# Optimization experiments

Hardware: AMD Instinct MI355X
Metric: run time of the kernel (lower is better)

## Reference

```python
import jax, jax.numpy as jnp
import numpy as np

EMB = 768
HEADS = 12
B, N = 8, 1024


def setup_inputs() -> dict:
    key = jax.random.key(0)
    ks = jax.random.split(key, 5)
    x = jax.random.normal(ks[0], (B, N, EMB), dtype=jnp.float32)
    # torch Linear params expressed as (in, out) matrices: y = x @ W + b
    W_qkv = jax.random.normal(ks[1], (EMB, 3 * EMB), dtype=jnp.float32) * (EMB ** -0.5)
    b_qkv = jax.random.normal(ks[2], (3 * EMB,), dtype=jnp.float32) * 0.02
    W_proj = jax.random.normal(ks[3], (EMB, EMB), dtype=jnp.float32) * (EMB ** -0.5)
    b_proj = jax.random.normal(ks[4], (EMB,), dtype=jnp.float32) * 0.02
    return {"x": x, "W_qkv": W_qkv, "b_qkv": b_qkv, "W_proj": W_proj, "b_proj": b_proj}


def reference(x, W_qkv, b_qkv, W_proj, b_proj):
    b, n, e = x.shape
    h = HEADS
    d = e // h
    qkv = x @ W_qkv + b_qkv                      # (b, n, 3e)
    # rearrange 'b n (h d qkv) -> qkv b h n d': qkv is the INNERMOST factor
    qkv = qkv.reshape(b, n, h, d, 3)
    q = jnp.transpose(qkv[..., 0], (0, 2, 1, 3))  # (b, h, n, d)
    k = jnp.transpose(qkv[..., 1], (0, 2, 1, 3))
    v = jnp.transpose(qkv[..., 2], (0, 2, 1, 3))
    energy = jnp.einsum('bhqd,bhkd->bhqk', q, k)  # UNscaled scores
    # faithful to source: softmax first, THEN divide by sqrt(emb_size)
    att = jax.nn.softmax(energy, axis=-1) / jnp.sqrt(jnp.float32(e))
    out = jnp.einsum('bhql,bhld->bhqd', att, v)   # (b, h, n, d)
    out = jnp.transpose(out, (0, 2, 1, 3)).reshape(b, n, e)
    return out @ W_proj + b_proj
```

## Files before the change

kernel.cpp:

```cpp
#include <hip/hip_runtime.h>
#include <hip/hip_bf16.h>
#include <stdint.h>

#define EMB 768
#define HEADS 12
#define BATCH 8
#define SEQ 1024
#define HD 64
#define M_ROWS (BATCH * SEQ)
#define QKV_COLS (3 * EMB)

typedef __attribute__((ext_vector_type(8))) short short8;
typedef __attribute__((ext_vector_type(4))) float f32x4;

__device__ __forceinline__ unsigned short f2bf(float x) {
    union { float f; unsigned u; } v; v.f = x;
    unsigned r = v.u + 0x7FFFu + ((v.u >> 16) & 1u);
    return (unsigned short)(r >> 16);
}
__device__ __forceinline__ float bf2f(unsigned short h) {
    union { unsigned u; float f; } v; v.u = ((unsigned)h) << 16;
    return v.f;
}
__device__ __forceinline__ float truncbf(float x) {
    return __uint_as_float(__float_as_uint(x) & 0xFFFF0000u);
}
__device__ __forceinline__ uint32_t packtr(float a, float b) {
    return (__float_as_uint(a) >> 16) | (__float_as_uint(b) & 0xFFFF0000u);
}
__device__ __forceinline__ uint32_t cvtpk(float a, float b) {
    uint32_t r;
    asm("v_cvt_pk_bf16_f32 %0, %1, %2" : "=v"(r) : "v"(a), "v"(b));
    return r;
}

#define MFMA16(a, b, c) __builtin_amdgcn_mfma_f32_16x16x32_bf16((a), (b), (c), 0, 0, 0)

__global__ __launch_bounds__(256)
void split_tw(const float* __restrict__ W,
              unsigned short* __restrict__ Wht, unsigned short* __restrict__ Wlt)
{
    __shared__ unsigned short Th[64][72], Tl[64][72];
    const int tid = threadIdx.x;
    const int ct = blockIdx.x * 64;
    const int kt = blockIdx.y * 64;

    #pragma unroll
    for (int p = 0; p < 4; ++p) {
        int idx = (p << 8) + tid;
        int k = idx >> 4, c4 = (idx & 15) << 2;
        f32x4 v = *reinterpret_cast<const f32x4*>(W + (size_t)(kt + k) * QKV_COLS + ct + c4);
        #pragma unroll
        for (int j = 0; j < 4; ++j) {
            const int whichj = (ct + c4 + j) % 3;
            if (whichj == 2) {
                Th[c4 + j][k] = f2bf(v[j]);
                Tl[c4 + j][k] = 0;
            } else {
                Th[c4 + j][k] = (unsigned short)(__float_as_uint(v[j]) >> 16);
                Tl[c4 + j][k] = (unsigned short)(__float_as_uint(v[j] - truncbf(v[j])) >> 16);
            }
        }
    }
    __syncthreads();
    #pragma unroll
    for (int p = 0; p < 2; ++p) {
        int idx = (p << 8) + tid;
        int c = idx >> 3, k8 = (idx & 7) << 3;
        const int s = ct + c;
        const int dst = (s % 3) * 768 + (s / 192) * 64 + (s % 192) / 3;
        *reinterpret_cast<uint4*>(Wht + (size_t)dst * EMB + kt + k8) =
            *reinterpret_cast<const uint4*>(&Th[c][k8]);
        *reinterpret_cast<uint4*>(Wlt + (size_t)dst * EMB + kt + k8) =
            *reinterpret_cast<const uint4*>(&Tl[c][k8]);
    }
}

__global__ __launch_bounds__(256, 2)
void gemm_qk(const float* __restrict__ X,
             const unsigned short* __restrict__ Wht, const unsigned short* __restrict__ Wlt,
             const float* __restrict__ bias,
             unsigned short* __restrict__ Qh, unsigned short* __restrict__ Ql,
             unsigned short* __restrict__ Kh, unsigned short* __restrict__ Kl)
{
    __shared__ unsigned short Ash[128][40], Asl[128][40];
    __shared__ unsigned short Bsh[128][40], Bsl[128][40];

    const int tid  = threadIdx.x;
    const int wave = tid >> 6, lane = tid & 63;
    const int lr = lane & 15, lg = lane >> 4;
    const int wr = (wave >> 1) * 64, wc = (wave & 1) * 64;
    const int m0 = blockIdx.y * 128;
    const int c0 = blockIdx.x * 128;

    const f32x4 fzero = {0.f, 0.f, 0.f, 0.f};
    f32x4 acc[4][4];
    #pragma unroll
    for (int m = 0; m < 4; ++m)
        #pragma unroll
        for (int n = 0; n < 4; ++n) acc[m][n] = fzero;

    for (int k0 = 0; k0 < EMB; k0 += 32) {
        #pragma unroll
        for (int p = 0; p < 4; ++p) {
            int idx = (p << 8) + tid;
            int row = idx >> 3, kc = (idx & 7) << 2;
            f32x4 v = *reinterpret_cast<const f32x4*>(X + (size_t)(m0 + row) * EMB + k0 + kc);
            float l0 = v[0] - truncbf(v[0]), l1 = v[1] - truncbf(v[1]);
            float l2 = v[2] - truncbf(v[2]), l3 = v[3] - truncbf(v[3]);
            uint2 hw = { packtr(v[0], v[1]), packtr(v[2], v[3]) };
            uint2 lw = { packtr(l0, l1), packtr(l2, l3) };
            *reinterpret_cast<uint2*>(&Ash[row][kc]) = hw;
            *reinterpret_cast<uint2*>(&Asl[row][kc]) = lw;
        }
        #pragma unroll
        for (int p = 0; p < 2; ++p) {
            int idx = (p << 8) + tid;
            int row = idx >> 2, kc = (idx & 3) << 3;
            const size_t boff = (size_t)(c0 + row) * EMB + k0 + kc;
            *reinterpret_cast<uint4*>(&Bsh[row][kc]) = *reinterpret_cast<const uint4*>(Wht + boff);
            *reinterpret_cast<uint4*>(&Bsl[row][kc]) = *reinterpret_cast<const uint4*>(Wlt + boff);
        }
        __syncthreads();

        short8 ah[4], al[4], bh[4], bl[4];
        #pragma unroll
        for (int m = 0; m < 4; ++m) {
            ah[m] = *reinterpret_cast<const short8*>(&Ash[wr + m * 16 + lr][lg << 3]);
            al[m] = *reinterpret_cast<const short8*>(&Asl[wr + m * 16 + lr][lg << 3]);
        }
        #pragma unroll
        for (int n = 0; n < 4; ++n) {
            bh[n] = *reinterpret_cast<const short8*>(&Bsh[wc + n * 16 + lr][lg << 3]);
            bl[n] = *reinterpret_cast<const short8*>(&Bsl[wc + n * 16 + lr][lg << 3]);
        }
        #pragma unroll
        for (int m = 0; m < 4; ++m)
            #pragma unroll
            for (int n = 0; n < 4; ++n) {
                acc[m][n] = MFMA16(ah[m], bh[n], acc[m][n]);
                acc[m][n] = MFMA16(ah[m], bl[n], acc[m][n]);
                acc[m][n] = MFMA16(al[m], bh[n], acc[m][n]);
            }
        __syncthreads();
    }

    const int which = c0 / 768;
    unsigned short* __restrict__ Ph = (which == 0) ? Qh : Kh;
    unsigned short* __restrict__ Pl = (which == 0) ? Ql : Kl;
    #pragma unroll
    for (int m = 0; m < 4; ++m) {
        #pragma unroll
        for (int n = 0; n < 4; ++n) {
            const int colg = c0 + wc + n * 16 + lr;
            const int hd = colg - which * 768;
            const int h  = hd >> 6;
            const int dd = hd & 63;
            const float bv = bias[192 * h + 3 * dd + which];
            const int rowg0 = m0 + wr + m * 16 + (lg << 2);
            const int bi = rowg0 >> 10, ni0 = rowg0 & (SEQ - 1);
            const int bhid = bi * HEADS + h;
            #pragma unroll
            for (int j = 0; j < 4; ++j) {
                const float val = acc[m][n][j] + bv;
                const size_t oidx = ((size_t)bhid * SEQ + ni0 + j) * HD + dd;
                const uint32_t uv = __float_as_uint(val);
                Ph[oidx] = (unsigned short)(uv >> 16);
                Pl[oidx] = (unsigned short)(__float_as_uint(
                    val - __uint_as_float(uv & 0xFFFF0000u)) >> 16);
            }
        }
    }
}

__global__ __launch_bounds__(256, 2)
void gemm_v(const float* __restrict__ X,
            const unsigned short* __restrict__ Wht,
            const float* __restrict__ bias,
            unsigned short* __restrict__ Vt)
{
    __shared__ unsigned short Ash[128][40];
    __shared__ unsigned short Bsh[128][40];

    const int tid  = threadIdx.x;
    const int wave = tid >> 6, lane = tid & 63;
    const int lr = lane & 15, lg = lane >> 4;
    const int wr = (wave >> 1) * 64, wc = (wave & 1) * 64;
    const int m0 = blockIdx.y * 128;
    const int c0 = blockIdx.x * 128;

    const f32x4 fzero = {0.f, 0.f, 0.f, 0.f};
    f32x4 acc[4][4];
    #pragma unroll
    for (int m = 0; m < 4; ++m)
        #pragma unroll
        for (int n = 0; n < 4; ++n) acc[m][n] = fzero;

    for (int k0 = 0; k0 < EMB; k0 += 32) {
        #pragma unroll
        for (int p = 0; p < 4; ++p) {
            int idx = (p << 8) + tid;
            int row = idx >> 3, kc = (idx & 7) << 2;
            f32x4 v = *reinterpret_cast<const f32x4*>(X + (size_t)(m0 + row) * EMB + k0 + kc);
            uint2 hw = { packtr(v[0], v[1]), packtr(v[2], v[3]) };
            *reinterpret_cast<uint2*>(&Ash[row][kc]) = hw;
        }
        #pragma unroll
        for (int p = 0; p < 2; ++p) {
            int idx = (p << 8) + tid;
            int row = idx >> 2, kc = (idx & 3) << 3;
            const size_t boff = (size_t)(1536 + c0 + row) * EMB + k0 + kc;
            *reinterpret_cast<uint4*>(&Bsh[row][kc]) = *reinterpret_cast<const uint4*>(Wht + boff);
        }
        __syncthreads();

        short8 a[4], b[4];
        #pragma unroll
        for (int m = 0; m < 4; ++m)
            a[m] = *reinterpret_cast<const short8*>(&Ash[wr + m * 16 + lr][lg << 3]);
        #pragma unroll
        for (int n = 0; n < 4; ++n)
            b[n] = *reinterpret_cast<const short8*>(&Bsh[wc + n * 16 + lr][lg << 3]);
        #pragma unroll
        for (int m = 0; m < 4; ++m)
            #pragma unroll
            for (int n = 0; n < 4; ++n)
                acc[m][n] = MFMA16(a[m], b[n], acc[m][n]);
        __syncthreads();
    }

    #pragma unroll
    for (int m = 0; m < 4; ++m) {
        #pragma unroll
        for (int n = 0; n < 4; ++n) {
            const int hd = c0 + wc + n * 16 + lr;
            const int h  = hd >> 6;
            const int dd = hd & 63;
            const float bv = bias[192 * h + 3 * dd + 2];
            const int rowg0 = m0 + wr + m * 16 + (lg << 2);
            const int bi = rowg0 >> 10, ni0 = rowg0 & (SEQ - 1);
            const int bhid = bi * HEADS + h;
            const float v0 = acc[m][n][0] + bv, v1 = acc[m][n][1] + bv;
            const float v2 = acc[m][n][2] + bv, v3 = acc[m][n][3] + bv;
            uint2 w = { (uint32_t)f2bf(v0) | ((uint32_t)f2bf(v1) << 16),
                        (uint32_t)f2bf(v2) | ((uint32_t)f2bf(v3) << 16) };
            *reinterpret_cast<uint2*>(Vt + ((size_t)bhid * HD + dd) * SEQ + ni0) = w;
        }
    }
}

__global__ __launch_bounds__(256, 4)
void attn_fused(const unsigned short* __restrict__ Qh, const unsigned short* __restrict__ Ql,
                const unsigned short* __restrict__ Kh, const unsigned short* __restrict__ Kl,
                const unsigned short* __restrict__ Vt,
                unsigned short* __restrict__ Ob)
{
    __shared__ unsigned short Vs[64][72];
    __shared__ unsigned short Ksh[64][72];
    __shared__ unsigned short Ksl[64][72];
    __shared__ unsigned short Plds[4][16][72];

    const int tid  = threadIdx.x;
    const int wave = tid >> 6, lane = tid & 63;
    const int lr = lane & 15, lg = lane >> 4;

    const int bid = blockIdx.x;
    const int lid = (bid & 7) * 192 + (bid >> 3);
    const int qt = lid & 15;
    const int bh = lid >> 4;
    const int b = bh / HEADS, h = bh % HEADS;

    const size_t base = (size_t)bh * SEQ * HD;
    const unsigned short* Qhb = Qh + base;
    const unsigned short* Qlb = Ql + base;
    const unsigned short* Khb = Kh + base;
    const unsigned short* Klb = Kl + base;
    const unsigned short* Vtb = Vt + base;

    const int q0 = qt * 64 + wave * 16;

    short8 qh[2], ql[2];
    #pragma unroll
    for (int kk = 0; kk < 2; ++kk) {
        const size_t off = (size_t)(q0 + lr) * HD + kk * 32 + (lg << 3);
        qh[kk] = *reinterpret_cast<const short8*>(Qhb + off);
        ql[kk] = *reinterpret_cast<const short8*>(Qlb + off);
    }

    const int r0 = tid >> 3, cs = (tid & 7) << 3;
    const int r1 = r0 + 32;

    uint4 vr0 = *reinterpret_cast<const uint4*>(Vtb + (size_t)r0 * SEQ + cs);
    uint4 vr1 = *reinterpret_cast<const uint4*>(Vtb + (size_t)r1 * SEQ + cs);
    uint4 kh0 = *reinterpret_cast<const uint4*>(Khb + (size_t)r0 * HD + cs);
    uint4 kh1 = *reinterpret_cast<const uint4*>(Khb + (size_t)r1 * HD + cs);
    uint4 kl0 = *reinterpret_cast<const uint4*>(Klb + (size_t)r0 * HD + cs);
    uint4 kl1 = *reinterpret_cast<const uint4*>(Klb + (size_t)r1 * HD + cs);

    float m = -1.0e30f, l = 0.f;
    f32x4 oacc[4];
    const f32x4 fzero = {0.f, 0.f, 0.f, 0.f};
    #pragma unroll
    for (int d = 0; d < 4; ++d) oacc[d] = fzero;

    for (int t = 0; t < SEQ / 64; ++t) {
        __syncthreads();
        *reinterpret_cast<uint4*>(&Vs[r0][cs])  = vr0;
        *reinterpret_cast<uint4*>(&Vs[r1][cs])  = vr1;
        *reinterpret_cast<uint4*>(&Ksh[r0][cs]) = kh0;
        *reinterpret_cast<uint4*>(&Ksh[r1][cs]) = kh1;
        *reinterpret_cast<uint4*>(&Ksl[r0][cs]) = kl0;
        *reinterpret_cast<uint4*>(&Ksl[r1][cs]) = kl1;
        __syncthreads();

        if (t < SEQ / 64 - 1) {
            const int kb = (t + 1) * 64;
            vr0 = *reinterpret_cast<const uint4*>(Vtb + (size_t)r0 * SEQ + kb + cs);
            vr1 = *reinterpret_cast<const uint4*>(Vtb + (size_t)r1 * SEQ + kb + cs);
            kh0 = *reinterpret_cast<const uint4*>(Khb + (size_t)(kb + r0) * HD + cs);
            kh1 = *reinterpret_cast<const uint4*>(Khb + (size_t)(kb + r1) * HD + cs);
            kl0 = *reinterpret_cast<const uint4*>(Klb + (size_t)(kb + r0) * HD + cs);
            kl1 = *reinterpret_cast<const uint4*>(Klb + (size_t)(kb + r1) * HD + cs);
        }

        f32x4 s[4];
        #pragma unroll
        for (int n = 0; n < 4; ++n) s[n] = fzero;
        #pragma unroll
        for (int n = 0; n < 4; ++n) {
            #pragma unroll
            for (int kk = 0; kk < 2; ++kk) {
                const short8 kh = *reinterpret_cast<const short8*>(&Ksh[n * 16 + lr][kk * 32 + (lg << 3)]);
                const short8 kl = *reinterpret_cast<const short8*>(&Ksl[n * 16 + lr][kk * 32 + (lg << 3)]);
                s[n] = MFMA16(kh, qh[kk], s[n]);
                s[n] = MFMA16(kh, ql[kk], s[n]);
                s[n] = MFMA16(kl, qh[kk], s[n]);
            }
        }

        float a0 = fmaxf(fmaxf(s[0][0], s[0][1]), s[0][2]);
        float a1 = fmaxf(fmaxf(s[0][3], s[1][0]), s[1][1]);
        float a2 = fmaxf(fmaxf(s[1][2], s[1][3]), s[2][0]);
        float a3 = fmaxf(fmaxf(s[2][1], s[2][2]), s[2][3]);
        float a4 = fmaxf(fmaxf(s[3][0], s[3][1]), s[3][2]);
        float tmax = fmaxf(fmaxf(fmaxf(a0, a1), a2), fmaxf(fmaxf(a3, a4), s[3][3]));
        tmax = fmaxf(tmax, __shfl_xor(tmax, 16));
        tmax = fmaxf(tmax, __shfl_xor(tmax, 32));

        if (!__all(tmax <= m + 8.0f)) {
            const float mnew = fmaxf(m, tmax);
            const float corr = __expf(m - mnew);
            m = mnew;
            l *= corr;
            #pragma unroll
            for (int j = 0; j < 4; ++j) {
                const float cj = __shfl(corr, (lg << 2) + j);
                oacc[0][j] *= cj; oacc[1][j] *= cj;
                oacc[2][j] *= cj; oacc[3][j] *= cj;
            }
        }

        float psum = 0.f;
        #pragma unroll
        for (int n = 0; n < 4; ++n) {
            const float p0 = __expf(s[n][0] - m), p1 = __expf(s[n][1] - m);
            const float p2 = __expf(s[n][2] - m), p3 = __expf(s[n][3] - m);
            psum += (p0 + p1) + (p2 + p3);
            uint2 w = { cvtpk(p0, p1), cvtpk(p2, p3) };
            *reinterpret_cast<uint2*>(&Plds[wave][lr][n * 16 + (lg << 2)]) = w;
        }
        psum += __shfl_xor(psum, 16);
        psum += __shfl_xor(psum, 32);
        l += psum;

        #pragma unroll
        for (int kk = 0; kk < 2; ++kk) {
            const short8 ap = *reinterpret_cast<const short8*>(&Plds[wave][lr][kk * 32 + (lg << 3)]);
            #pragma unroll
            for (int d = 0; d < 4; ++d) {
                const short8 bv = *reinterpret_cast<const short8*>(&Vs[d * 16 + lr][kk * 32 + (lg << 3)]);
                oacc[d] = MFMA16(ap, bv, oacc[d]);
            }
        }
    }

    const float rs = 0.036084391824351615f;
    #pragma unroll
    for (int j = 0; j < 4; ++j) {
        const float lj = __shfl(l, (lg << 2) + j);
        const float sc = rs / lj;
        const int q = q0 + (lg << 2) + j;
        #pragma unroll
        for (int d = 0; d < 4; ++d) {
            const float val = oacc[d][j] * sc;
            Ob[((size_t)b * SEQ + q) * EMB + h * HD + d * 16 + lr] = f2bf(val);
        }
    }
}

__global__ __launch_bounds__(256, 4)
void gemm_proj(const unsigned short* __restrict__ A, const float* __restrict__ W,
               const float* __restrict__ bias, float* __restrict__ Out)
{
    __shared__ unsigned short As[128][40];
    __shared__ unsigned short Bs[128][40];

    const int tid  = threadIdx.x;
    const int wave = tid >> 6, lane = tid & 63;
    const int lr = lane & 15, lg = lane >> 4;
    const int wr = (wave >> 1) * 64, wc = (wave & 1) * 64;
    const int m0 = blockIdx.y * 128;
    const int c0 = blockIdx.x * 128;

    const f32x4 fzero = {0.f, 0.f, 0.f, 0.f};
    f32x4 acc[4][4];
    #pragma unroll
    for (int m = 0; m < 4; ++m)
        #pragma unroll
        for (int n = 0; n < 4; ++n) acc[m][n] = fzero;

    const int kgB = tid & 7, cgB = tid >> 3;

    for (int k0 = 0; k0 < EMB; k0 += 32) {
        #pragma unroll
        for (int p = 0; p < 2; ++p) {
            int idx = (p << 8) + tid;
            int row = idx >> 2, kc = (idx & 3) << 3;
            uint4 v = *reinterpret_cast<const uint4*>(A + (size_t)(m0 + row) * EMB + k0 + kc);
            *reinterpret_cast<uint4*>(&As[row][kc]) = v;
        }
        {
            f32x4 v[4];
            #pragma unroll
            for (int i = 0; i < 4; ++i)
                v[i] = *reinterpret_cast<const f32x4*>(
                    W + (size_t)(k0 + kgB * 4 + i) * EMB + c0 + cgB * 4);
            #pragma unroll
            for (int j = 0; j < 4; ++j) {
                uint2 w = { (uint32_t)f2bf(v[0][j]) | ((uint32_t)f2bf(v[1][j]) << 16),
                            (uint32_t)f2bf(v[2][j]) | ((uint32_t)f2bf(v[3][j]) << 16) };
                *reinterpret_cast<uint2*>(&Bs[cgB * 4 + j][kgB * 4]) = w;
            }
        }
        __syncthreads();

        short8 a[4], b[4];
        #pragma unroll
        for (int m = 0; m < 4; ++m)
            a[m] = *reinterpret_cast<const short8*>(&As[wr + m * 16 + lr][lg << 3]);
        #pragma unroll
        for (int n = 0; n < 4; ++n)
            b[n] = *reinterpret_cast<const short8*>(&Bs[wc + n * 16 + lr][lg << 3]);
        #pragma unroll
        for (int m = 0; m < 4; ++m)
            #pragma unroll
            for (int n = 0; n < 4; ++n)
                acc[m][n] = MFMA16(a[m], b[n], acc[m][n]);
        __syncthreads();
    }

    #pragma unroll
    for (int m = 0; m < 4; ++m) {
        #pragma unroll
        for (int n = 0; n < 4; ++n) {
            const int colg = c0 + wc + n * 16 + lr;
            const float bv = bias[colg];
            #pragma unroll
            for (int j = 0; j < 4; ++j) {
                const int rowg = m0 + wr + m * 16 + (lg << 2) + j;
                Out[(size_t)rowg * EMB + colg] = acc[m][n][j] + bv;
            }
        }
    }
}

extern "C" void kernel_launch(void* const* d_in, const int* in_sizes, int n_in,
                              void* d_out, int out_size, void* d_ws, size_t ws_size,
                              hipStream_t stream)
{
    const float* x     = (const float*)d_in[0];
    const float* Wqkv  = (const float*)d_in[1];
    const float* bqkv  = (const float*)d_in[2];
    const float* Wproj = (const float*)d_in[3];
    const float* bproj = (const float*)d_in[4];
    float* out = (float*)d_out;

    const size_t NQ = (size_t)BATCH * HEADS * SEQ * HD;
    const size_t NW = (size_t)EMB * QKV_COLS;

    unsigned short* Qh = (unsigned short*)d_ws;
    unsigned short* Ql = Qh + NQ;
    unsigned short* Kh = Ql + NQ;
    unsigned short* Kl = Kh + NQ;
    unsigned short* Vt = Kl + NQ;
    unsigned short* Ob = Vt + NQ;

    unsigned short* Wht = Ob;
    unsigned short* Wlt = Wht + NW;

    split_tw<<<dim3(QKV_COLS / 64, EMB / 64), 256, 0, stream>>>(Wqkv, Wht, Wlt);
    gemm_qk<<<dim3(1536 / 128, M_ROWS / 128), 256, 0, stream>>>(
        x, Wht, Wlt, bqkv, Qh, Ql, Kh, Kl);
    gemm_v<<<dim3(768 / 128, M_ROWS / 128), 256, 0, stream>>>(
        x, Wht, bqkv, Vt);
    attn_fused<<<dim3(16 * BATCH * HEADS), 256, 0, stream>>>(Qh, Ql, Kh, Kl, Vt, Ob);
    gemm_proj<<<dim3(EMB / 128, M_ROWS / 128), 256, 0, stream>>>(
        Ob, Wproj, bproj, out);
}
```

Baseline: 207.0 us.

## Process two query tiles per attention block and double QK GEMM K-step

The attention kernel now handles 128 queries per block as two 64-query sub-tiles, so each K/V tile staged in shared memory is reused by twice as many queries and the grid is halved. Each sub-tile keeps its own online-softmax state and P buffer. The QK projection GEMM moves from 32 to 64 k-elements per iteration with larger LDS tiles, which halves the number of barrier pairs. In exchange both kernels use more registers and LDS, occupancy drops (attention launch bounds go from 4 to 3), and the attention grid has fewer blocks to spread across the CUs.

Result: no change. 210.9 us (+1.9%).

```diff
diff --git a/kernel.cpp b/kernel.cpp
--- a/kernel.cpp
+++ b/kernel.cpp
@@ -83,8 +83,8 @@
              unsigned short* __restrict__ Qh, unsigned short* __restrict__ Ql,
              unsigned short* __restrict__ Kh, unsigned short* __restrict__ Kl)
 {
-    __shared__ unsigned short Ash[128][40], Asl[128][40];
-    __shared__ unsigned short Bsh[128][40], Bsl[128][40];
+    __shared__ unsigned short Ash[128][72], Asl[128][72];
+    __shared__ unsigned short Bsh[128][72], Bsl[128][72];
 
     const int tid  = threadIdx.x;
     const int wave = tid >> 6, lane = tid & 63;
@@ -100,11 +100,11 @@
         #pragma unroll
         for (int n = 0; n < 4; ++n) acc[m][n] = fzero;
 
-    for (int k0 = 0; k0 < EMB; k0 += 32) {
-        #pragma unroll
-        for (int p = 0; p < 4; ++p) {
+    for (int k0 = 0; k0 < EMB; k0 += 64) {
+        #pragma unroll
+        for (int p = 0; p < 8; ++p) {
             int idx = (p << 8) + tid;
-            int row = idx >> 3, kc = (idx & 7) << 2;
+            int row = idx >> 4, kc = (idx & 15) << 2;
             f32x4 v = *reinterpret_cast<const f32x4*>(X + (size_t)(m0 + row) * EMB + k0 + kc);
             float l0 = v[0] - truncbf(v[0]), l1 = v[1] - truncbf(v[1]);
             float l2 = v[2] - truncbf(v[2]), l3 = v[3] - truncbf(v[3]);
@@ -114,34 +114,37 @@
             *reinterpret_cast<uint2*>(&Asl[row][kc]) = lw;
         }
         #pragma unroll
-        for (int p = 0; p < 2; ++p) {
+        for (int p = 0; p < 4; ++p) {
             int idx = (p << 8) + tid;
-            int row = idx >> 2, kc = (idx & 3) << 3;
+            int row = idx >> 3, kc = (idx & 7) << 3;
             const size_t boff = (size_t)(c0 + row) * EMB + k0 + kc;
             *reinterpret_cast<uint4*>(&Bsh[row][kc]) = *reinterpret_cast<const uint4*>(Wht + boff);
             *reinterpret_cast<uint4*>(&Bsl[row][kc]) = *reinterpret_cast<const uint4*>(Wlt + boff);
         }
         __syncthreads();
 
-        short8 ah[4], al[4], bh[4], bl[4];
-        #pragma unroll
-        for (int m = 0; m < 4; ++m) {
-            ah[m] = *reinterpret_cast<const short8*>(&Ash[wr + m * 16 + lr][lg << 3]);
-            al[m] = *reinterpret_cast<const short8*>(&Asl[wr + m * 16 + lr][lg << 3]);
-        }
-        #pragma unroll
-        for (int n = 0; n < 4; ++n) {
-            bh[n] = *reinterpret_cast<const short8*>(&Bsh[wc + n * 16 + lr][lg << 3]);
-            bl[n] = *reinterpret_cast<const short8*>(&Bsl[wc + n * 16 + lr][lg << 3]);
-        }
-        #pragma unroll
-        for (int m = 0; m < 4; ++m)
+        #pragma unroll
+        for (int kk = 0; kk < 2; ++kk) {
+            short8 ah[4], al[4], bh[4], bl[4];
+            #pragma unroll
+            for (int m = 0; m < 4; ++m) {
+                ah[m] = *reinterpret_cast<const short8*>(&Ash[wr + m * 16 + lr][kk * 32 + (lg << 3)]);
+                al[m] = *reinterpret_cast<const short8*>(&Asl[wr + m * 16 + lr][kk * 32 + (lg << 3)]);
+            }
             #pragma unroll
             for (int n = 0; n < 4; ++n) {
-                acc[m][n] = MFMA16(ah[m], bh[n], acc[m][n]);
-                acc[m][n] = MFMA16(ah[m], bl[n], acc[m][n]);
-                acc[m][n] = MFMA16(al[m], bh[n], acc[m][n]);
-            }
+                bh[n] = *reinterpret_cast<const short8*>(&Bsh[wc + n * 16 + lr][kk * 32 + (lg << 3)]);
+                bl[n] = *reinterpret_cast<const short8*>(&Bsl[wc + n * 16 + lr][kk * 32 + (lg << 3)]);
+            }
+            #pragma unroll
+            for (int m = 0; m < 4; ++m)
+                #pragma unroll
+                for (int n = 0; n < 4; ++n) {
+                    acc[m][n] = MFMA16(ah[m], bh[n], acc[m][n]);
+                    acc[m][n] = MFMA16(ah[m], bl[n], acc[m][n]);
+                    acc[m][n] = MFMA16(al[m], bh[n], acc[m][n]);
+                }
+        }
         __syncthreads();
     }
 
@@ -249,7 +252,7 @@
     }
 }
 
-__global__ __launch_bounds__(256, 4)
+__global__ __launch_bounds__(256, 3)
 void attn_fused(const unsigned short* __restrict__ Qh, const unsigned short* __restrict__ Ql,
                 const unsigned short* __restrict__ Kh, const unsigned short* __restrict__ Kl,
                 const unsigned short* __restrict__ Vt,
@@ -258,16 +261,16 @@
     __shared__ unsigned short Vs[64][72];
     __shared__ unsigned short Ksh[64][72];
     __shared__ unsigned short Ksl[64][72];
-    __shared__ unsigned short Plds[4][16][72];
+    __shared__ unsigned short Plds[2][4][16][72];
 
     const int tid  = threadIdx.x;
     const int wave = tid >> 6, lane = tid & 63;
     const int lr = lane & 15, lg = lane >> 4;
 
     const int bid = blockIdx.x;
-    const int lid = (bid & 7) * 192 + (bid >> 3);
-    const int qt = lid & 15;
-    const int bh = lid >> 4;
+    const int lid = (bid & 7) * 96 + (bid >> 3);
+    const int qt = lid & 7;
+    const int bh = lid >> 3;
     const int b = bh / HEADS, h = bh % HEADS;
 
     const size_t base = (size_t)bh * SEQ * HD;
@@ -277,14 +280,18 @@
     const unsigned short* Klb = Kl + base;
     const unsigned short* Vtb = Vt + base;
 
-    const int q0 = qt * 64 + wave * 16;
-
-    short8 qh[2], ql[2];
+    const int qA = qt * 128 + wave * 16;
+    const int qB = qA + 64;
+
+    short8 qhA[2], qlA[2], qhB[2], qlB[2];
     #pragma unroll
     for (int kk = 0; kk < 2; ++kk) {
-        const size_t off = (size_t)(q0 + lr) * HD + kk * 32 + (lg << 3);
-        qh[kk] = *reinterpret_cast<const short8*>(Qhb + off);
-        ql[kk] = *reinterpret_cast<const short8*>(Qlb + off);
+        const size_t offA = (size_t)(qA + lr) * HD + kk * 32 + (lg << 3);
+        const size_t offB = (size_t)(qB + lr) * HD + kk * 32 + (lg << 3);
+        qhA[kk] = *reinterpret_cast<const short8*>(Qhb + offA);
+        qlA[kk] = *reinterpret_cast<const short8*>(Qlb + offA);
+        qhB[kk] = *reinterpret_cast<const short8*>(Qhb + offB);
+        qlB[kk] = *reinterpret_cast<const short8*>(Qlb + offB);
     }
 
     const int r0 = tid >> 3, cs = (tid & 7) << 3;
@@ -297,11 +304,11 @@
     uint4 kl0 = *reinterpret_cast<const uint4*>(Klb + (size_t)r0 * HD + cs);
     uint4 kl1 = *reinterpret_cast<const uint4*>(Klb + (size_t)r1 * HD + cs);
 
-    float m = -1.0e30f, l = 0.f;
-    f32x4 oacc[4];
+    float mA = -1.0e30f, lA = 0.f, mB = -1.0e30f, lB = 0.f;
+    f32x4 oaccA[4], oaccB[4];
     const f32x4 fzero = {0.f, 0.f, 0.f, 0.f};
     #pragma unroll
-    for (int d = 0; d < 4; ++d) oacc[d] = fzero;
+    for (int d = 0; d < 4; ++d) { oaccA[d] = fzero; oaccB[d] = fzero; }
 
     for (int t = 0; t < SEQ / 64; ++t) {
         __syncthreads();
@@ -323,63 +330,109 @@
             kl1 = *reinterpret_cast<const uint4*>(Klb + (size_t)(kb + r1) * HD + cs);
         }
 
-        f32x4 s[4];
-        #pragma unroll
-        for (int n = 0; n < 4; ++n) s[n] = fzero;
+        f32x4 sA[4], sB[4];
+        #pragma unroll
+        for (int n = 0; n < 4; ++n) { sA[n] = fzero; sB[n] = fzero; }
         #pragma unroll
         for (int n = 0; n < 4; ++n) {
             #pragma unroll
             for (int kk = 0; kk < 2; ++kk) {
                 const short8 kh = *reinterpret_cast<const short8*>(&Ksh[n * 16 + lr][kk * 32 + (lg << 3)]);
                 const short8 kl = *reinterpret_cast<const short8*>(&Ksl[n * 16 + lr][kk * 32 + (lg << 3)]);
-                s[n] = MFMA16(kh, qh[kk], s[n]);
-                s[n] = MFMA16(kh, ql[kk], s[n]);
-                s[n] = MFMA16(kl, qh[kk], s[n]);
-            }
-        }
-
-        float a0 = fmaxf(fmaxf(s[0][0], s[0][1]), s[0][2]);
-        float a1 = fmaxf(fmaxf(s[0][3], s[1][0]), s[1][1]);
-        float a2 = fmaxf(fmaxf(s[1][2], s[1][3]), s[2][0]);
-        float a3 = fmaxf(fmaxf(s[2][1], s[2][2]), s[2][3]);
-        float a4 = fmaxf(fmaxf(s[3][0], s[3][1]), s[3][2]);
-        float tmax = fmaxf(fmaxf(fmaxf(a0, a1), a2), fmaxf(fmaxf(a3, a4), s[3][3]));
-        tmax = fmaxf(tmax, __shfl_xor(tmax, 16));
-        tmax = fmaxf(tmax, __shfl_xor(tmax, 32));
-
-        if (!__all(tmax <= m + 8.0f)) {
-            const float mnew = fmaxf(m, tmax);
-            const float corr = __expf(m - mnew);
-            m = mnew;
-            l *= corr;
-            #pragma unroll
-            for (int j = 0; j < 4; ++j) {
-                const float cj = __shfl(corr, (lg << 2) + j);
-                oacc[0][j] *= cj; oacc[1][j] *= cj;
-                oacc[2][j] *= cj; oacc[3][j] *= cj;
-            }
-        }
-
-        float psum = 0.f;
-        #pragma unroll
-        for (int n = 0; n < 4; ++n) {
-            const float p0 = __expf(s[n][0] - m), p1 = __expf(s[n][1] - m);
-            const float p2 = __expf(s[n][2] - m), p3 = __expf(s[n][3] - m);
-            psum += (p0 + p1) + (p2 + p3);
-            uint2 w = { cvtpk(p0, p1), cvtpk(p2, p3) };
-            *reinterpret_cast<uint2*>(&Plds[wave][lr][n * 16 + (lg << 2)]) = w;
-        }
-        psum += __shfl_xor(psum, 16);
-        psum += __shfl_xor(psum, 32);
-        l += psum;
-
-        #pragma unroll
-        for (int kk = 0; kk < 2; ++kk) {
-            const short8 ap = *reinterpret_cast<const short8*>(&Plds[wave][lr][kk * 32 + (lg << 3)]);
-            #pragma unroll
-            for (int d = 0; d < 4; ++d) {
-                const short8 bv = *reinterpret_cast<const short8*>(&Vs[d * 16 + lr][kk * 32 + (lg << 3)]);
-                oacc[d] = MFMA16(ap, bv, oacc[d]);
+                sA[n] = MFMA16(kh, qhA[kk], sA[n]);
+                sA[n] = MFMA16(kh, qlA[kk], sA[n]);
+                sA[n] = MFMA16(kl, qhA[kk], sA[n]);
+                sB[n] = MFMA16(kh, qhB[kk], sB[n]);
+                sB[n] = MFMA16(kh, qlB[kk], sB[n]);
+                sB[n] = MFMA16(kl, qhB[kk], sB[n]);
+            }
+        }
+
+        {
+            float a0 = fmaxf(fmaxf(sA[0][0], sA[0][1]), sA[0][2]);
+            float a1 = fmaxf(fmaxf(sA[0][3], sA[1][0]), sA[1][1]);
+            float a2 = fmaxf(fmaxf(sA[1][2], sA[1][3]), sA[2][0]);
+            float a3 = fmaxf(fmaxf(sA[2][1], sA[2][2]), sA[2][3]);
+            float a4 = fmaxf(fmaxf(sA[3][0], sA[3][1]), sA[3][2]);
+            float tmax = fmaxf(fmaxf(fmaxf(a0, a1), a2), fmaxf(fmaxf(a3, a4), sA[3][3]));
+            tmax = fmaxf(tmax, __shfl_xor(tmax, 16));
+            tmax = fmaxf(tmax, __shfl_xor(tmax, 32));
+            if (!__all(tmax <= mA + 8.0f)) {
+                const float mnew = fmaxf(mA, tmax);
+                const float corr = __expf(mA - mnew);
+                mA = mnew;
+                lA *= corr;
+                #pragma unroll
+                for (int j = 0; j < 4; ++j) {
+                    const float cj = __shfl(corr, (lg << 2) + j);
+                    oaccA[0][j] *= cj; oaccA[1][j] *= cj;
+                    oaccA[2][j] *= cj; oaccA[3][j] *= cj;
+                }
+            }
+            float psum = 0.f;
+            #pragma unroll
+            for (int n = 0; n < 4; ++n) {
+                const float p0 = __expf(sA[n][0] - mA), p1 = __expf(sA[n][1] - mA);
+                const float p2 = __expf(sA[n][2] - mA), p3 = __expf(sA[n][3] - mA);
+                psum += (p0 + p1) + (p2 + p3);
+                uint2 w = { cvtpk(p0, p1), cvtpk(p2, p3) };
+                *reinterpret_cast<uint2*>(&Plds[0][wave][lr][n * 16 + (lg << 2)]) = w;
+            }
+            psum += __shfl_xor(psum, 16);
+            psum += __shfl_xor(psum, 32);
+            lA += psum;
+            #pragma unroll
+            for (int kk = 0; kk < 2; ++kk) {
+                const short8 ap = *reinterpret_cast<const short8*>(&Plds[0][wave][lr][kk * 32 + (lg << 3)]);
+                #pragma unroll
+                for (int d = 0; d < 4; ++d) {
+                    const short8 bv = *reinterpret_cast<const short8*>(&Vs[d * 16 + lr][kk * 32 + (lg << 3)]);
+                    oaccA[d] = MFMA16(ap, bv, oaccA[d]);
+                }
+            }
+        }
+
+        {
+            float a0 = fmaxf(fmaxf(sB[0][0], sB[0][1]), sB[0][2]);
+            float a1 = fmaxf(fmaxf(sB[0][3], sB[1][0]), sB[1][1]);
+            float a2 = fmaxf(fmaxf(sB[1][2], sB[1][3]), sB[2][0]);
+            float a3 = fmaxf(fmaxf(sB[2][1], sB[2][2]), sB[2][3]);
+            float a4 = fmaxf(fmaxf(sB[3][0], sB[3][1]), sB[3][2]);
+            float tmax = fmaxf(fmaxf(fmaxf(a0, a1), a2), fmaxf(fmaxf(a3, a4), sB[3][3]));
+            tmax = fmaxf(tmax, __shfl_xor(tmax, 16));
+            tmax = fmaxf(tmax, __shfl_xor(tmax, 32));
+            if (!__all(tmax <= mB + 8.0f)) {
+                const float mnew = fmaxf(mB, tmax);
+                const float corr = __expf(mB - mnew);
+                mB = mnew;
+                lB *= corr;
+                #pragma unroll
+                for (int j = 0; j < 4; ++j) {
+                    const float cj = __shfl(corr, (lg << 2) + j);
+                    oaccB[0][j] *= cj; oaccB[1][j] *= cj;
+                    oaccB[2][j] *= cj; oaccB[3][j] *= cj;
+                }
+            }
+            float psum = 0.f;
+            #pragma unroll
+            for (int n = 0; n < 4; ++n) {
+                const float p0 = __expf(sB[n][0] - mB), p1 = __expf(sB[n][1] - mB);
+                const float p2 = __expf(sB[n][2] - mB), p3 = __expf(sB[n][3] - mB);
+                psum += (p0 + p1) + (p2 + p3);
+                uint2 w = { cvtpk(p0, p1), cvtpk(p2, p3) };
+                *reinterpret_cast<uint2*>(&Plds[1][wave][lr][n * 16 + (lg << 2)]) = w;
+            }
+            psum += __shfl_xor(psum, 16);
+            psum += __shfl_xor(psum, 32);
+            lB += psum;
+            #pragma unroll
+            for (int kk = 0; kk < 2; ++kk) {
+                const short8 ap = *reinterpret_cast<const short8*>(&Plds[1][wave][lr][kk * 32 + (lg << 3)]);
+                #pragma unroll
+                for (int d = 0; d < 4; ++d) {
+                    const short8 bv = *reinterpret_cast<const short8*>(&Vs[d * 16 + lr][kk * 32 + (lg << 3)]);
+                    oaccB[d] = MFMA16(ap, bv, oaccB[d]);
+                }
             }
         }
     }
@@ -387,13 +440,16 @@
     const float rs = 0.036084391824351615f;
     #pragma unroll
     for (int j = 0; j < 4; ++j) {
-        const float lj = __shfl(l, (lg << 2) + j);
-        const float sc = rs / lj;
-        const int q = q0 + (lg << 2) + j;
+        const float ljA = __shfl(lA, (lg << 2) + j);
+        const float ljB = __shfl(lB, (lg << 2) + j);
+        const float scA = rs / ljA;
+        const float scB = rs / ljB;
+        const int qa = qA + (lg << 2) + j;
+        const int qb = qB + (lg << 2) + j;
         #pragma unroll
         for (int d = 0; d < 4; ++d) {
-            const float val = oacc[d][j] * sc;
-            Ob[((size_t)b * SEQ + q) * EMB + h * HD + d * 16 + lr] = f2bf(val);
+            Ob[((size_t)b * SEQ + qa) * EMB + h * HD + d * 16 + lr] = f2bf(oaccA[d][j] * scA);
+            Ob[((size_t)b * SEQ + qb) * EMB + h * HD + d * 16 + lr] = f2bf(oaccB[d][j] * scB);
         }
     }
 }
@@ -503,7 +559,7 @@
         x, Wht, Wlt, bqkv, Qh, Ql, Kh, Kl);
     gemm_v<<<dim3(768 / 128, M_ROWS / 128), 256, 0, stream>>>(
         x, Wht, bqkv, Vt);
-    attn_fused<<<dim3(16 * BATCH * HEADS), 256, 0, stream>>>(Qh, Ql, Kh, Kl, Vt, Ob);
+    attn_fused<<<dim3(8 * BATCH * HEADS), 256, 0, stream>>>(Qh, Ql, Kh, Kl, Vt, Ob);
     gemm_proj<<<dim3(EMB / 128, M_ROWS / 128), 256, 0, stream>>>(
         Ob, Wproj, bproj, out);
 }
```
